# Kernel optimization log

Hardware: AMD Instinct MI355X
Metric: run time of the kernel (lower is better)

## Reference

```python
import jax, jax.numpy as jnp
import numpy as np

H_NODE = 256
H_EDGE = 64
B = 8        # number of graphs
A_PER = 64   # anchors per graph
N_PER = 512  # nodes per graph
INF = 1000000.0
EPS = 1e-8
D_MIN, D_MAX = 0.0, 20.0  # _rbf defaults (gvp-style)


def setup_inputs() -> dict:
    key = jax.random.key(0)
    ks = jax.random.split(key, 16)
    h, he = H_NODE, H_EDGE
    n = lambda k, shp, s=1.0: jax.random.normal(k, shp, jnp.float32) * s
    return {
        "anchor_x": n(ks[0], (B * A_PER, 3), 10.0),
        "node_x": n(ks[1], (B * N_PER, 3), 10.0),
        "anchor_features": n(ks[2], (B * A_PER, h)),
        "node_features": n(ks[3], (B * N_PER, h)),
        "batch": jnp.repeat(jnp.arange(B, dtype=jnp.int32), N_PER),
        "anchor_batch": jnp.repeat(jnp.arange(B, dtype=jnp.int32), A_PER),
        "node_mask": (jax.random.uniform(ks[4], (B * N_PER,)) < 0.9).astype(jnp.float32),
        "Wq": n(ks[5], (h, h), h ** -0.5), "bq": jnp.zeros((h,), jnp.float32),
        "Wkv": n(ks[6], (2 * h, h + he), (h + he) ** -0.5), "bkv": jnp.zeros((2 * h,), jnp.float32),
        "ln1_g": jnp.ones((h,), jnp.float32), "ln1_b": jnp.zeros((h,), jnp.float32),
        "W1": n(ks[7], (2 * h, h), h ** -0.5), "b1": jnp.zeros((2 * h,), jnp.float32),
        "W2": n(ks[8], (2 * h, 2 * h), (2 * h) ** -0.5), "b2": jnp.zeros((2 * h,), jnp.float32),
        "W3": n(ks[9], (h, 2 * h), (2 * h) ** -0.5), "b3": jnp.zeros((h,), jnp.float32),
        "ln2_g": jnp.ones((h,), jnp.float32), "ln2_b": jnp.zeros((h,), jnp.float32),
    }


def _ln(x, g, b, eps=1e-5):
    m = x.mean(-1, keepdims=True)
    v = ((x - m) ** 2).mean(-1, keepdims=True)
    return (x - m) * jax.lax.rsqrt(v + eps) * g + b


def _forward(anchor_x, node_x, anchor_features, node_features, node_mask,
             Wq, bq, Wkv, bkv, ln1_g, ln1_b, W1, b1, W2, b2, W3, b3, ln2_g, ln2_b):
    h, he = H_NODE, H_EDGE
    # equal-sized graphs: reshape global tensors to [B, ., .] (batch ids are repeat(arange(B)))
    q = (anchor_features @ Wq.T + bq).reshape(B, A_PER, h)
    ax = anchor_x.reshape(B, A_PER, 3)
    nx = node_x.reshape(B, N_PER, 3)
    nf = node_features.reshape(B, N_PER, h)
    mask = node_mask.reshape(B, N_PER)

    # pairwise anchor->node distances; original adds scalar eps to the diff vector before the norm
    dist = jnp.linalg.norm(ax[:, :, None, :] - nx[:, None, :, :] + EPS, axis=-1)  # [B,A,N]

    # RBF featurization of dist/10 with D_count = h_edge
    mu = jnp.linspace(D_MIN, D_MAX, he)
    sigma = (D_MAX - D_MIN) / he
    rbf = jnp.exp(-(((dist / 10.0)[..., None] - mu) / sigma) ** 2)  # [B,A,N,he]

    # kv_node(cat([node_feat, rbf])) decomposed: node part computed once per node
    Wkv_n, Wkv_e = Wkv[:, :h], Wkv[:, h:]
    kv_n = nf @ Wkv_n.T + bkv                 # [B,N,2h]
    kv_e = rbf @ Wkv_e.T                      # [B,A,N,2h]
    kv = kv_n[:, None, :, :] + kv_e           # [B,A,N,2h]
    k, v = kv[..., :h], kv[..., h:]

    attn = jnp.einsum('bah,banh->ban', q, k)
    attn = attn * ((mask[:, None, :] - 1.0) * INF)  # faithful to original (multiplicative mask)
    attn = jax.nn.softmax(attn, axis=-1)
    upd = jnp.einsum('ban,banh->bah', attn, v).reshape(B * A_PER, h)

    af = _ln(anchor_features + upd, ln1_g, ln1_b)
    m = jax.nn.relu(af @ W1.T + b1)
    m = jax.nn.relu(m @ W2.T + b2)
    m = m @ W3.T + b3
    return _ln(af + m, ln2_g, ln2_b)


def reference(anchor_x, node_x, anchor_features, node_features, batch, anchor_batch, node_mask,
              Wq, bq, Wkv, bkv, ln1_g, ln1_b, W1, b1, W2, b2, W3, b3, ln2_g, ln2_b):
    # batch / anchor_batch encode equal-sized contiguous graphs; structure is baked into reshapes
    return _forward(anchor_x, node_x, anchor_features, node_features, node_mask,
                    Wq, bq, Wkv, bkv, ln1_g, ln1_b, W1, b1, W2, b2, W3, b3, ln2_g, ln2_b)
```

## Files before the change

kernel.cpp:

```cpp
#include <hip/hip_runtime.h>

#define H    256
#define HE   64
#define NPB  512
#define NA   512
#define MU_STEP (20.0f / 63.0f)
#define INV_SIG 3.2f

__device__ __forceinline__ float wave_sum(float v) {
#pragma unroll
    for (int o = 32; o; o >>= 1) v += __shfl_xor(v, o, 64);
    return v;
}
__device__ __forceinline__ float wave_max(float v) {
#pragma unroll
    for (int o = 32; o; o >>= 1) v = fmaxf(v, __shfl_xor(v, o, 64));
    return v;
}
__device__ __forceinline__ float block_sum1024(float v, float* red16, int t) {
    v = wave_sum(v);
    if ((t & 63) == 0) red16[t >> 6] = v;
    __syncthreads();
    v = 0.f;
#pragma unroll
    for (int i = 0; i < 16; ++i) v += red16[i];
    __syncthreads();
    return v;
}

__global__ void __launch_bounds__(1024) fused_all(
    const float* __restrict__ anchor_x, const float* __restrict__ node_x,
    const float* __restrict__ anchor_f, const float* __restrict__ node_f,
    const float* __restrict__ node_mask,
    const float* __restrict__ Wq,  const float* __restrict__ bq,
    const float* __restrict__ Wkv, const float* __restrict__ bkv,
    const float* __restrict__ ln1_g, const float* __restrict__ ln1_b,
    const float* __restrict__ W1, const float* __restrict__ b1,
    const float* __restrict__ W2, const float* __restrict__ b2,
    const float* __restrict__ W3, const float* __restrict__ b3,
    const float* __restrict__ g2,  const float* __restrict__ bb2,
    float* __restrict__ out)
{
    const int bid = blockIdx.x;
    const int b  = bid & 7;
    const int pr = bid >> 3;
    const int aA = b * 64 + 2 * pr;
    const int aB = aA + 1;
    const int t  = threadIdx.x;
    const int wv = t >> 6, l = t & 63;
    const int sub = l >> 4, kc16 = l & 15;

    __shared__ __align__(16) float qWe_s[2][324];
    __shared__ float q_s[2][256];
    __shared__ float af_s[2][256];
    __shared__ float d10_s[2][NPB];
    __shared__ float mf_s[NPB];
    __shared__ float lg_s[2][NPB];
    __shared__ float w_s[2][NPB];
    __shared__ float snf_s[2][256], rj_s[2][64];
    __shared__ float m1_s[2][512], m2_s[2][512];
    __shared__ float red[512], red16[16];
    __shared__ int   idx_s[2][NPB];
    __shared__ int   cnt_s[2];

    if (t < 256)       af_s[0][t]        = anchor_f[(size_t)aA * 256 + t];
    else if (t < 512)  af_s[1][t - 256]  = anchor_f[(size_t)aB * 256 + (t - 256)];
    if (t < 2) cnt_s[t] = 0;

    if (t < 512) {
        float axA0 = anchor_x[3 * aA], axA1 = anchor_x[3 * aA + 1], axA2 = anchor_x[3 * aA + 2];
        float axB0 = anchor_x[3 * aB], axB1 = anchor_x[3 * aB + 1], axB2 = anchor_x[3 * aB + 2];
        int ng = b * NPB + t;
        float nx0 = node_x[3 * ng], nx1 = node_x[3 * ng + 1], nx2 = node_x[3 * ng + 2];
        float dx = axA0 - nx0 + 1e-8f, dy = axA1 - nx1 + 1e-8f, dz = axA2 - nx2 + 1e-8f;
        d10_s[0][t] = sqrtf(dx * dx + dy * dy + dz * dz) * 0.1f;
        dx = axB0 - nx0 + 1e-8f; dy = axB1 - nx1 + 1e-8f; dz = axB2 - nx2 + 1e-8f;
        d10_s[1][t] = sqrtf(dx * dx + dy * dy + dz * dz) * 0.1f;
        mf_s[t] = (node_mask[ng] - 1.0f) * 1000000.0f;
    }
    __syncthreads();

#pragma unroll
    for (int pass = 0; pass < 4; ++pass) {
        int m = pass * 64 + wv * 4 + sub;
        const float* wr = Wq + (size_t)m * 256 + kc16;
        float w16[16];
#pragma unroll
        for (int v = 0; v < 16; ++v) w16[v] = wr[v * 16];
        float aAc = 0.f, aBc = 0.f;
#pragma unroll
        for (int v = 0; v < 16; ++v) {
            int c = kc16 + v * 16;
            aAc = fmaf(w16[v], af_s[0][c], aAc);
            aBc = fmaf(w16[v], af_s[1][c], aBc);
        }
#pragma unroll
        for (int o = 8; o >= 1; o >>= 1) {
            aAc += __shfl_xor(aAc, o, 64);
            aBc += __shfl_xor(aBc, o, 64);
        }
        if (kc16 == 0) {
            float bv = bq[m];
            q_s[0][m] = aAc + bv;
            q_s[1][m] = aBc + bv;
        }
    }
    __syncthreads();

    {
        int ha = -1, col = 0;
        if (t < 320)                   { ha = 0; col = t; }
        else if (t >= 512 && t < 832)  { ha = 1; col = t - 512; }
        if (ha >= 0) {
            const float* qs = q_s[ha];
            float acc = 0.f;
            for (int o = 0; o < 256; o += 16) {
                float w16[16];
#pragma unroll
                for (int u = 0; u < 16; ++u) w16[u] = Wkv[(size_t)(o + u) * 320 + col];
#pragma unroll
                for (int u = 0; u < 16; ++u) acc = fmaf(w16[u], qs[o + u], acc);
            }
            qWe_s[ha][col] = acc;
        }
    }
    float qbkA = block_sum1024((t < 256) ? q_s[0][t] * bkv[t] : 0.f, red16, t);
    float qbkB = block_sum1024((t < 256) ? q_s[1][t] * bkv[t] : 0.f, red16, t);

    {
        const float4 qA = ((const float4*)qWe_s[0])[l];
        const float4 qB = ((const float4*)qWe_s[1])[l];
        const float qeA = qWe_s[0][256 + l], qeB = qWe_s[1][256 + l];
        const float muL = l * MU_STEP;
        const float4* nfb = (const float4*)(node_f + (size_t)(b * NPB) * 256);

        float4 f0 = nfb[(size_t)wv * 64 + l];
        float4 f1 = nfb[(size_t)(wv + 16) * 64 + l];
        for (int it = 0; it < 32; ++it) {
            const int n = wv + it * 16;
            float4 fn;
            if (it < 30) fn = nfb[(size_t)(n + 32) * 64 + l];

            float sA = qA.x * f0.x + qA.y * f0.y + qA.z * f0.z + qA.w * f0.w;
            float sB = qB.x * f0.x + qB.y * f0.y + qB.z * f0.z + qB.w * f0.w;
            float dA10 = d10_s[0][n], dB10 = d10_s[1][n];
            float u = (dA10 - muL) * INV_SIG; sA = fmaf(qeA, __expf(-u * u), sA);
            u = (dB10 - muL) * INV_SIG;       sB = fmaf(qeB, __expf(-u * u), sB);
#pragma unroll
            for (int o = 1; o < 64; o <<= 1) {
                sA += __shfl_xor(sA, o, 64);
                sB += __shfl_xor(sB, o, 64);
            }
            if (l == 0) {
                lg_s[0][n] = (sA + qbkA) * mf_s[n];
                lg_s[1][n] = (sB + qbkB) * mf_s[n];
            }
            f0 = f1; f1 = fn;
        }
    }
    __syncthreads();

    const int h8 = t >> 9, n9 = t & 511;
    float lg = lg_s[h8][n9];
    {
        float m = wave_max(lg);
        if (l == 0) red16[wv] = m;
    }
    __syncthreads();
    float gmA = red16[0], gmB = red16[8];
#pragma unroll
    for (int i = 1; i < 8; ++i) { gmA = fmaxf(gmA, red16[i]); gmB = fmaxf(gmB, red16[8 + i]); }
    __syncthreads();
    float e = __expf(lg - (h8 ? gmB : gmA));
    w_s[h8][n9] = e;
    {
        float sm = wave_sum(e);
        if (l == 0) red16[wv] = sm;
    }
    __syncthreads();
    float smA = 0.f, smB = 0.f;
#pragma unroll
    for (int i = 0; i < 8; ++i) { smA += red16[i]; smB += red16[8 + i]; }
    const float invA = 1.0f / smA, invB = 1.0f / smB;
    if (e > 0.f) { int p = atomicAdd(&cnt_s[h8], 1); idx_s[h8][p] = n9; }
    __syncthreads();

    if (t < 512) {
        const int hh = t >> 8, col = t & 255;
        const int cnt = cnt_s[hh];
        float s = 0.f;
        const float* base = node_f + (size_t)(b * NPB) * 256 + col;
        for (int i = 0; i < cnt; ++i) {
            int n = idx_s[hh][i];
            s += w_s[hh][n] * base[(size_t)n * 256];
        }
        snf_s[hh][col] = s;
    } else {
        const int tt = t - 512;
        const int ha = tt >> 8, j = tt & 63, g = (tt >> 6) & 3;
        const int cnt = cnt_s[ha];
        float mu = j * MU_STEP;
        float r = 0.f;
        for (int i = g; i < cnt; i += 4) {
            int n = idx_s[ha][i];
            float uu = (d10_s[ha][n] - mu) * INV_SIG;
            r += w_s[ha][n] * __expf(-uu * uu);
        }
        red[tt] = r;
    }
    __syncthreads();
    if (t < 128) {
        int ha = t >> 6, j = t & 63;
        rj_s[ha][j] = red[ha * 256 + j] + red[ha * 256 + 64 + j]
                    + red[ha * 256 + 128 + j] + red[ha * 256 + 192 + j];
    }
    __syncthreads();

#pragma unroll
    for (int pass = 0; pass < 4; ++pass) {
        int m = pass * 64 + wv * 4 + sub;
        const float* wr = Wkv + (size_t)(256 + m) * 320 + kc16;
        float w16[16], w4r[4];
#pragma unroll
        for (int v = 0; v < 16; ++v) w16[v] = wr[v * 16];
#pragma unroll
        for (int v = 0; v < 4; ++v) w4r[v] = wr[256 + v * 16];
        float aAc = 0.f, aBc = 0.f;
#pragma unroll
        for (int v = 0; v < 16; ++v) {
            int c = kc16 + v * 16;
            aAc = fmaf(w16[v], snf_s[0][c], aAc);
            aBc = fmaf(w16[v], snf_s[1][c], aBc);
        }
#pragma unroll
        for (int v = 0; v < 4; ++v) {
            int j = kc16 + v * 16;
            aAc = fmaf(w4r[v], rj_s[0][j], aAc);
            aBc = fmaf(w4r[v], rj_s[1][j], aBc);
        }
#pragma unroll
        for (int o = 8; o >= 1; o >>= 1) {
            aAc += __shfl_xor(aAc, o, 64);
            aBc += __shfl_xor(aBc, o, 64);
        }
        if (kc16 == 0) { red[m] = aAc; red[256 + m] = aBc; }
    }
    __syncthreads();

    const int h = (t >> 8) & 1, th = t & 255;
    float x = 0.f;
    if (t < 512)
        x = af_s[h][th] + red[h * 256 + th] * (h ? invB : invA) + bkv[256 + th];
    {
        float s1 = wave_sum(x);
        if (l == 0) red16[wv] = s1;
    }
    __syncthreads();
    float meanA = (red16[0] + red16[1] + red16[2] + red16[3]) * (1.0f / 256.0f);
    float meanB = (red16[4] + red16[5] + red16[6] + red16[7]) * (1.0f / 256.0f);
    __syncthreads();
    float xc = (t < 512) ? (x - (h ? meanB : meanA)) : 0.f;
    {
        float v1 = wave_sum(xc * xc);
        if (l == 0) red16[wv] = v1;
    }
    __syncthreads();
    float varA = (red16[0] + red16[1] + red16[2] + red16[3]) * (1.0f / 256.0f);
    float varB = (red16[4] + red16[5] + red16[6] + red16[7]) * (1.0f / 256.0f);
    __syncthreads();
    if (t < 512)
        af_s[h][th] = xc * rsqrtf((h ? varB : varA) + 1e-5f) * ln1_g[th] + ln1_b[th];
    __syncthreads();

#pragma unroll
    for (int pass = 0; pass < 8; ++pass) {
        int m = pass * 64 + wv * 4 + sub;
        const float* wr = W1 + (size_t)m * 256 + kc16;
        float w16[16];
#pragma unroll
        for (int v = 0; v < 16; ++v) w16[v] = wr[v * 16];
        float aAc = 0.f, aBc = 0.f;
#pragma unroll
        for (int v = 0; v < 16; ++v) {
            int c = kc16 + v * 16;
            aAc = fmaf(w16[v], af_s[0][c], aAc);
            aBc = fmaf(w16[v], af_s[1][c], aBc);
        }
#pragma unroll
        for (int o = 8; o >= 1; o >>= 1) {
            aAc += __shfl_xor(aAc, o, 64);
            aBc += __shfl_xor(aBc, o, 64);
        }
        if (kc16 == 0) {
            float bv = b1[m];
            m1_s[0][m] = fmaxf(aAc + bv, 0.f);
            m1_s[1][m] = fmaxf(aBc + bv, 0.f);
        }
    }
    __syncthreads();

#pragma unroll
    for (int pass = 0; pass < 8; ++pass) {
        int m = pass * 64 + wv * 4 + sub;
        const float* wr = W2 + (size_t)m * 512 + kc16;
        float aAc = 0.f, aBc = 0.f;
#pragma unroll
        for (int u = 0; u < 32; u += 16) {
            float w16[16];
#pragma unroll
            for (int v = 0; v < 16; ++v) w16[v] = wr[(u + v) * 16];
#pragma unroll
            for (int v = 0; v < 16; ++v) {
                int c = kc16 + (u + v) * 16;
                aAc = fmaf(w16[v], m1_s[0][c], aAc);
                aBc = fmaf(w16[v], m1_s[1][c], aBc);
            }
        }
#pragma unroll
        for (int o = 8; o >= 1; o >>= 1) {
            aAc += __shfl_xor(aAc, o, 64);
            aBc += __shfl_xor(aBc, o, 64);
        }
        if (kc16 == 0) {
            float bv = b2[m];
            m2_s[0][m] = fmaxf(aAc + bv, 0.f);
            m2_s[1][m] = fmaxf(aBc + bv, 0.f);
        }
    }
    __syncthreads();

#pragma unroll
    for (int pass = 0; pass < 4; ++pass) {
        int m = pass * 64 + wv * 4 + sub;
        const float* wr = W3 + (size_t)m * 512 + kc16;
        float aAc = 0.f, aBc = 0.f;
#pragma unroll
        for (int u = 0; u < 32; u += 16) {
            float w16[16];
#pragma unroll
            for (int v = 0; v < 16; ++v) w16[v] = wr[(u + v) * 16];
#pragma unroll
            for (int v = 0; v < 16; ++v) {
                int c = kc16 + (u + v) * 16;
                aAc = fmaf(w16[v], m2_s[0][c], aAc);
                aBc = fmaf(w16[v], m2_s[1][c], aBc);
            }
        }
#pragma unroll
        for (int o = 8; o >= 1; o >>= 1) {
            aAc += __shfl_xor(aAc, o, 64);
            aBc += __shfl_xor(aBc, o, 64);
        }
        if (kc16 == 0) {
            float bv = b3[m];
            red[m]       = aAc + bv;
            red[256 + m] = aBc + bv;
        }
    }
    __syncthreads();

    float y = 0.f;
    if (t < 512) y = red[h * 256 + th] + af_s[h][th];
    {
        float s1 = wave_sum(y);
        if (l == 0) red16[wv] = s1;
    }
    __syncthreads();
    float mnA = (red16[0] + red16[1] + red16[2] + red16[3]) * (1.0f / 256.0f);
    float mnB = (red16[4] + red16[5] + red16[6] + red16[7]) * (1.0f / 256.0f);
    __syncthreads();
    float yc = (t < 512) ? (y - (h ? mnB : mnA)) : 0.f;
    {
        float v1 = wave_sum(yc * yc);
        if (l == 0) red16[wv] = v1;
    }
    __syncthreads();
    float vrA = (red16[0] + red16[1] + red16[2] + red16[3]) * (1.0f / 256.0f);
    float vrB = (red16[4] + red16[5] + red16[6] + red16[7]) * (1.0f / 256.0f);
    if (t < 512) {
        int aOut = h ? aB : aA;
        out[(size_t)aOut * 256 + th] =
            yc * rsqrtf((h ? vrB : vrA) + 1e-5f) * g2[th] + bb2[th];
    }
}

extern "C" void kernel_launch(void* const* d_in, const int* in_sizes, int n_in,
                              void* d_out, int out_size, void* d_ws, size_t ws_size,
                              hipStream_t stream)
{
    const float* anchor_x  = (const float*)d_in[0];
    const float* node_x    = (const float*)d_in[1];
    const float* anchor_f  = (const float*)d_in[2];
    const float* node_f    = (const float*)d_in[3];
    const float* node_mask = (const float*)d_in[6];
    const float* Wq        = (const float*)d_in[7];
    const float* bq        = (const float*)d_in[8];
    const float* Wkv       = (const float*)d_in[9];
    const float* bkv       = (const float*)d_in[10];
    const float* ln1_g     = (const float*)d_in[11];
    const float* ln1_b     = (const float*)d_in[12];
    const float* W1        = (const float*)d_in[13];
    const float* b1        = (const float*)d_in[14];
    const float* W2        = (const float*)d_in[15];
    const float* b2        = (const float*)d_in[16];
    const float* W3        = (const float*)d_in[17];
    const float* b3        = (const float*)d_in[18];
    const float* ln2_g     = (const float*)d_in[19];
    const float* ln2_b     = (const float*)d_in[20];

    fused_all<<<256, 1024, 0, stream>>>(anchor_x, node_x, anchor_f, node_f,
                                        node_mask, Wq, bq, Wkv, bkv,
                                        ln1_g, ln1_b, W1, b1, W2, b2, W3, b3,
                                        ln2_g, ln2_b, (float*)d_out);
}
```

Before: 164.5 us.

## Process one anchor per block and launch 512 blocks instead of 256

Each block previously handled two anchors that shared weight and node-feature loads. Now each block handles a single anchor and the grid doubles to 512 blocks, which fills more of the GPU's compute units (256 CUs on MI355X) at the cost of re-reading the weights and node features twice as often. Shared-memory use per block shrinks, and the launch bounds now request 8 waves per SIMD, which may cap registers per thread. Half of the threads sit idle in several phases, such as the 256-wide layer norms and gathers.

```diff
diff --git a/kernel.cpp b/kernel.cpp
--- a/kernel.cpp
+++ b/kernel.cpp
@@ -28,7 +28,7 @@
     return v;
 }
 
-__global__ void __launch_bounds__(1024) fused_all(
+__global__ void __launch_bounds__(1024, 8) fused_all(
     const float* __restrict__ anchor_x, const float* __restrict__ node_x,
     const float* __restrict__ anchor_f, const float* __restrict__ node_f,
     const float* __restrict__ node_mask,
@@ -42,41 +42,36 @@
     float* __restrict__ out)
 {
     const int bid = blockIdx.x;
-    const int b  = bid & 7;
-    const int pr = bid >> 3;
-    const int aA = b * 64 + 2 * pr;
-    const int aB = aA + 1;
+    const int b = bid & 7;
+    const int a = b * 64 + (bid >> 3);
     const int t  = threadIdx.x;
     const int wv = t >> 6, l = t & 63;
     const int sub = l >> 4, kc16 = l & 15;
 
-    __shared__ __align__(16) float qWe_s[2][324];
-    __shared__ float q_s[2][256];
-    __shared__ float af_s[2][256];
-    __shared__ float d10_s[2][NPB];
+    __shared__ __align__(16) float qWe_s[324];
+    __shared__ float q_s[256];
+    __shared__ float af_s[256];
+    __shared__ float d10_s[NPB];
     __shared__ float mf_s[NPB];
-    __shared__ float lg_s[2][NPB];
-    __shared__ float w_s[2][NPB];
-    __shared__ float snf_s[2][256], rj_s[2][64];
-    __shared__ float m1_s[2][512], m2_s[2][512];
+    __shared__ float lg_s[NPB];
+    __shared__ float w_s[NPB];
+    __shared__ float snf_s[256], rj_s[64];
+    __shared__ float m1_s[512], m2_s[512];
     __shared__ float red[512], red16[16];
-    __shared__ int   idx_s[2][NPB];
-    __shared__ int   cnt_s[2];
-
-    if (t < 256)       af_s[0][t]        = anchor_f[(size_t)aA * 256 + t];
-    else if (t < 512)  af_s[1][t - 256]  = anchor_f[(size_t)aB * 256 + (t - 256)];
-    if (t < 2) cnt_s[t] = 0;
+    __shared__ int   idx_s[NPB];
+    __shared__ int   cnt_s;
+
+    if (t < 256) af_s[t] = anchor_f[(size_t)a * 256 + t];
+    if (t == 0) cnt_s = 0;
 
     if (t < 512) {
-        float axA0 = anchor_x[3 * aA], axA1 = anchor_x[3 * aA + 1], axA2 = anchor_x[3 * aA + 2];
-        float axB0 = anchor_x[3 * aB], axB1 = anchor_x[3 * aB + 1], axB2 = anchor_x[3 * aB + 2];
+        float ax0 = anchor_x[3 * a], ax1 = anchor_x[3 * a + 1], ax2 = anchor_x[3 * a + 2];
         int ng = b * NPB + t;
-        float nx0 = node_x[3 * ng], nx1 = node_x[3 * ng + 1], nx2 = node_x[3 * ng + 2];
-        float dx = axA0 - nx0 + 1e-8f, dy = axA1 - nx1 + 1e-8f, dz = axA2 - nx2 + 1e-8f;
-        d10_s[0][t] = sqrtf(dx * dx + dy * dy + dz * dz) * 0.1f;
-        dx = axB0 - nx0 + 1e-8f; dy = axB1 - nx1 + 1e-8f; dz = axB2 - nx2 + 1e-8f;
-        d10_s[1][t] = sqrtf(dx * dx + dy * dy + dz * dz) * 0.1f;
-        mf_s[t] = (node_mask[ng] - 1.0f) * 1000000.0f;
+        float dx = ax0 - node_x[3 * ng]     + 1e-8f;
+        float dy = ax1 - node_x[3 * ng + 1] + 1e-8f;
+        float dz = ax2 - node_x[3 * ng + 2] + 1e-8f;
+        d10_s[t] = sqrtf(dx * dx + dy * dy + dz * dz) * 0.1f;
+        mf_s[t]  = (node_mask[ng] - 1.0f) * 1000000.0f;
     }
     __syncthreads();
 
@@ -87,50 +82,31 @@
         float w16[16];
 #pragma unroll
         for (int v = 0; v < 16; ++v) w16[v] = wr[v * 16];
-        float aAc = 0.f, aBc = 0.f;
-#pragma unroll
-        for (int v = 0; v < 16; ++v) {
-            int c = kc16 + v * 16;
-            aAc = fmaf(w16[v], af_s[0][c], aAc);
-            aBc = fmaf(w16[v], af_s[1][c], aBc);
-        }
-#pragma unroll
-        for (int o = 8; o >= 1; o >>= 1) {
-            aAc += __shfl_xor(aAc, o, 64);
-            aBc += __shfl_xor(aBc, o, 64);
-        }
-        if (kc16 == 0) {
-            float bv = bq[m];
-            q_s[0][m] = aAc + bv;
-            q_s[1][m] = aBc + bv;
-        }
-    }
-    __syncthreads();
+        float acc = 0.f;
+#pragma unroll
+        for (int v = 0; v < 16; ++v) acc = fmaf(w16[v], af_s[kc16 + v * 16], acc);
+#pragma unroll
+        for (int o = 8; o >= 1; o >>= 1) acc += __shfl_xor(acc, o, 64);
+        if (kc16 == 0) q_s[m] = acc + bq[m];
+    }
+    __syncthreads();
+
+    if (t < 320) {
+        float acc = 0.f;
+        for (int o = 0; o < 256; o += 16) {
+            float w16[16];
+#pragma unroll
+            for (int u = 0; u < 16; ++u) w16[u] = Wkv[(size_t)(o + u) * 320 + t];
+#pragma unroll
+            for (int u = 0; u < 16; ++u) acc = fmaf(w16[u], q_s[o + u], acc);
+        }
+        qWe_s[t] = acc;
+    }
+    const float qbk = block_sum1024((t < 256) ? q_s[t] * bkv[t] : 0.f, red16, t);
 
     {
-        int ha = -1, col = 0;
-        if (t < 320)                   { ha = 0; col = t; }
-        else if (t >= 512 && t < 832)  { ha = 1; col = t - 512; }
-        if (ha >= 0) {
-            const float* qs = q_s[ha];
-            float acc = 0.f;
-            for (int o = 0; o < 256; o += 16) {
-                float w16[16];
-#pragma unroll
-                for (int u = 0; u < 16; ++u) w16[u] = Wkv[(size_t)(o + u) * 320 + col];
-#pragma unroll
-                for (int u = 0; u < 16; ++u) acc = fmaf(w16[u], qs[o + u], acc);
-            }
-            qWe_s[ha][col] = acc;
-        }
-    }
-    float qbkA = block_sum1024((t < 256) ? q_s[0][t] * bkv[t] : 0.f, red16, t);
-    float qbkB = block_sum1024((t < 256) ? q_s[1][t] * bkv[t] : 0.f, red16, t);
-
-    {
-        const float4 qA = ((const float4*)qWe_s[0])[l];
-        const float4 qB = ((const float4*)qWe_s[1])[l];
-        const float qeA = qWe_s[0][256 + l], qeB = qWe_s[1][256 + l];
+        const float4 qA = ((const float4*)qWe_s)[l];
+        const float qeA = qWe_s[256 + l];
         const float muL = l * MU_STEP;
         const float4* nfb = (const float4*)(node_f + (size_t)(b * NPB) * 256);
 
@@ -142,77 +118,68 @@
             if (it < 30) fn = nfb[(size_t)(n + 32) * 64 + l];
 
             float sA = qA.x * f0.x + qA.y * f0.y + qA.z * f0.z + qA.w * f0.w;
-            float sB = qB.x * f0.x + qB.y * f0.y + qB.z * f0.z + qB.w * f0.w;
-            float dA10 = d10_s[0][n], dB10 = d10_s[1][n];
-            float u = (dA10 - muL) * INV_SIG; sA = fmaf(qeA, __expf(-u * u), sA);
-            u = (dB10 - muL) * INV_SIG;       sB = fmaf(qeB, __expf(-u * u), sB);
-#pragma unroll
-            for (int o = 1; o < 64; o <<= 1) {
-                sA += __shfl_xor(sA, o, 64);
-                sB += __shfl_xor(sB, o, 64);
-            }
-            if (l == 0) {
-                lg_s[0][n] = (sA + qbkA) * mf_s[n];
-                lg_s[1][n] = (sB + qbkB) * mf_s[n];
-            }
+            float dA10 = d10_s[n];
+            float u = (dA10 - muL) * INV_SIG;
+            sA = fmaf(qeA, __expf(-u * u), sA);
+#pragma unroll
+            for (int o = 1; o < 64; o <<= 1) sA += __shfl_xor(sA, o, 64);
+            if (l == 0) lg_s[n] = (sA + qbk) * mf_s[n];
             f0 = f1; f1 = fn;
         }
     }
     __syncthreads();
 
-    const int h8 = t >> 9, n9 = t & 511;
-    float lg = lg_s[h8][n9];
+    float lg = (t < 512) ? lg_s[t] : -3.4e38f;
     {
         float m = wave_max(lg);
         if (l == 0) red16[wv] = m;
     }
     __syncthreads();
-    float gmA = red16[0], gmB = red16[8];
-#pragma unroll
-    for (int i = 1; i < 8; ++i) { gmA = fmaxf(gmA, red16[i]); gmB = fmaxf(gmB, red16[8 + i]); }
-    __syncthreads();
-    float e = __expf(lg - (h8 ? gmB : gmA));
-    w_s[h8][n9] = e;
+    float gm = red16[0];
+#pragma unroll
+    for (int i = 1; i < 16; ++i) gm = fmaxf(gm, red16[i]);
+    __syncthreads();
+    float e = (t < 512) ? __expf(lg - gm) : 0.f;
+    if (t < 512) w_s[t] = e;
     {
         float sm = wave_sum(e);
         if (l == 0) red16[wv] = sm;
     }
     __syncthreads();
-    float smA = 0.f, smB = 0.f;
-#pragma unroll
-    for (int i = 0; i < 8; ++i) { smA += red16[i]; smB += red16[8 + i]; }
-    const float invA = 1.0f / smA, invB = 1.0f / smB;
-    if (e > 0.f) { int p = atomicAdd(&cnt_s[h8], 1); idx_s[h8][p] = n9; }
-    __syncthreads();
-
-    if (t < 512) {
-        const int hh = t >> 8, col = t & 255;
-        const int cnt = cnt_s[hh];
+    float sm = 0.f;
+#pragma unroll
+    for (int i = 0; i < 16; ++i) sm += red16[i];
+    const float inv = 1.0f / sm;
+    if (t < 512 && e > 0.f) { int p = atomicAdd(&cnt_s, 1); idx_s[p] = t; }
+    __syncthreads();
+    const int cnt = cnt_s;
+
+    if (t < 256) {
         float s = 0.f;
-        const float* base = node_f + (size_t)(b * NPB) * 256 + col;
+        const float* base = node_f + (size_t)(b * NPB) * 256 + t;
         for (int i = 0; i < cnt; ++i) {
-            int n = idx_s[hh][i];
-            s += w_s[hh][n] * base[(size_t)n * 256];
-        }
-        snf_s[hh][col] = s;
-    } else {
+            int n = idx_s[i];
+            s += w_s[n] * base[(size_t)n * 256];
+        }
+        snf_s[t] = s;
+    } else if (t >= 512) {
         const int tt = t - 512;
-        const int ha = tt >> 8, j = tt & 63, g = (tt >> 6) & 3;
-        const int cnt = cnt_s[ha];
+        const int j = tt & 63, g = tt >> 6;
         float mu = j * MU_STEP;
         float r = 0.f;
-        for (int i = g; i < cnt; i += 4) {
-            int n = idx_s[ha][i];
-            float uu = (d10_s[ha][n] - mu) * INV_SIG;
-            r += w_s[ha][n] * __expf(-uu * uu);
+        for (int i = g; i < cnt; i += 8) {
+            int n = idx_s[i];
+            float uu = (d10_s[n] - mu) * INV_SIG;
+            r += w_s[n] * __expf(-uu * uu);
         }
         red[tt] = r;
     }
     __syncthreads();
-    if (t < 128) {
-        int ha = t >> 6, j = t & 63;
-        rj_s[ha][j] = red[ha * 256 + j] + red[ha * 256 + 64 + j]
-                    + red[ha * 256 + 128 + j] + red[ha * 256 + 192 + j];
+    if (t < 64) {
+        float r = 0.f;
+#pragma unroll
+        for (int g = 0; g < 8; ++g) r += red[t + 64 * g];
+        rj_s[t] = r;
     }
     __syncthreads();
 
@@ -225,51 +192,24 @@
         for (int v = 0; v < 16; ++v) w16[v] = wr[v * 16];
 #pragma unroll
         for (int v = 0; v < 4; ++v) w4r[v] = wr[256 + v * 16];
-        float aAc = 0.f, aBc = 0.f;
-#pragma unroll
-        for (int v = 0; v < 16; ++v) {
-            int c = kc16 + v * 16;
-            aAc = fmaf(w16[v], snf_s[0][c], aAc);
-            aBc = fmaf(w16[v], snf_s[1][c], aBc);
-        }
-#pragma unroll
-        for (int v = 0; v < 4; ++v) {
-            int j = kc16 + v * 16;
-            aAc = fmaf(w4r[v], rj_s[0][j], aAc);
-            aBc = fmaf(w4r[v], rj_s[1][j], aBc);
-        }
-#pragma unroll
-        for (int o = 8; o >= 1; o >>= 1) {
-            aAc += __shfl_xor(aAc, o, 64);
-            aBc += __shfl_xor(aBc, o, 64);
-        }
-        if (kc16 == 0) { red[m] = aAc; red[256 + m] = aBc; }
-    }
-    __syncthreads();
-
-    const int h = (t >> 8) & 1, th = t & 255;
+        float acc = 0.f;
+#pragma unroll
+        for (int v = 0; v < 16; ++v) acc = fmaf(w16[v], snf_s[kc16 + v * 16], acc);
+#pragma unroll
+        for (int v = 0; v < 4; ++v) acc = fmaf(w4r[v], rj_s[kc16 + v * 16], acc);
+#pragma unroll
+        for (int o = 8; o >= 1; o >>= 1) acc += __shfl_xor(acc, o, 64);
+        if (kc16 == 0) red[m] = acc;
+    }
+    __syncthreads();
+
     float x = 0.f;
-    if (t < 512)
-        x = af_s[h][th] + red[h * 256 + th] * (h ? invB : invA) + bkv[256 + th];
-    {
-        float s1 = wave_sum(x);
-        if (l == 0) red16[wv] = s1;
-    }
-    __syncthreads();
-    float meanA = (red16[0] + red16[1] + red16[2] + red16[3]) * (1.0f / 256.0f);
-    float meanB = (red16[4] + red16[5] + red16[6] + red16[7]) * (1.0f / 256.0f);
-    __syncthreads();
-    float xc = (t < 512) ? (x - (h ? meanB : meanA)) : 0.f;
-    {
-        float v1 = wave_sum(xc * xc);
-        if (l == 0) red16[wv] = v1;
-    }
-    __syncthreads();
-    float varA = (red16[0] + red16[1] + red16[2] + red16[3]) * (1.0f / 256.0f);
-    float varB = (red16[4] + red16[5] + red16[6] + red16[7]) * (1.0f / 256.0f);
-    __syncthreads();
-    if (t < 512)
-        af_s[h][th] = xc * rsqrtf((h ? varB : varA) + 1e-5f) * ln1_g[th] + ln1_b[th];
+    if (t < 256) x = af_s[t] + red[t] * inv + bkv[256 + t];
+    float mean = block_sum1024(x, red16, t) * (1.0f / 256.0f);
+    float xc = (t < 256) ? (x - mean) : 0.f;
+    float var = block_sum1024(xc * xc, red16, t) * (1.0f / 256.0f);
+    if (t < 256)
+        af_s[t] = xc * rsqrtf(var + 1e-5f) * ln1_g[t] + ln1_b[t];
     __syncthreads();
 
 #pragma unroll
@@ -279,23 +219,12 @@
         float w16[16];
 #pragma unroll
         for (int v = 0; v < 16; ++v) w16[v] = wr[v * 16];
-        float aAc = 0.f, aBc = 0.f;
-#pragma unroll
-        for (int v = 0; v < 16; ++v) {
-            int c = kc16 + v * 16;
-            aAc = fmaf(w16[v], af_s[0][c], aAc);
-            aBc = fmaf(w16[v], af_s[1][c], aBc);
-        }
-#pragma unroll
-        for (int o = 8; o >= 1; o >>= 1) {
-            aAc += __shfl_xor(aAc, o, 64);
-            aBc += __shfl_xor(aBc, o, 64);
-        }
-        if (kc16 == 0) {
-            float bv = b1[m];
-            m1_s[0][m] = fmaxf(aAc + bv, 0.f);
-            m1_s[1][m] = fmaxf(aBc + bv, 0.f);
-        }
+        float acc = 0.f;
+#pragma unroll
+        for (int v = 0; v < 16; ++v) acc = fmaf(w16[v], af_s[kc16 + v * 16], acc);
+#pragma unroll
+        for (int o = 8; o >= 1; o >>= 1) acc += __shfl_xor(acc, o, 64);
+        if (kc16 == 0) m1_s[m] = fmaxf(acc + b1[m], 0.f);
     }
     __syncthreads();
 
@@ -303,29 +232,19 @@
     for (int pass = 0; pass < 8; ++pass) {
         int m = pass * 64 + wv * 4 + sub;
         const float* wr = W2 + (size_t)m * 512 + kc16;
-        float aAc = 0.f, aBc = 0.f;
+        float acc = 0.f;
 #pragma unroll
         for (int u = 0; u < 32; u += 16) {
             float w16[16];
 #pragma unroll
             for (int v = 0; v < 16; ++v) w16[v] = wr[(u + v) * 16];
 #pragma unroll
-            for (int v = 0; v < 16; ++v) {
-                int c = kc16 + (u + v) * 16;
-                aAc = fmaf(w16[v], m1_s[0][c], aAc);
-                aBc = fmaf(w16[v], m1_s[1][c], aBc);
-            }
-        }
-#pragma unroll
-        for (int o = 8; o >= 1; o >>= 1) {
-            aAc += __shfl_xor(aAc, o, 64);
-            aBc += __shfl_xor(aBc, o, 64);
-        }
-        if (kc16 == 0) {
-            float bv = b2[m];
-            m2_s[0][m] = fmaxf(aAc + bv, 0.f);
-            m2_s[1][m] = fmaxf(aBc + bv, 0.f);
-        }
+            for (int v = 0; v < 16; ++v)
+                acc = fmaf(w16[v], m1_s[kc16 + (u + v) * 16], acc);
+        }
+#pragma unroll
+        for (int o = 8; o >= 1; o >>= 1) acc += __shfl_xor(acc, o, 64);
+        if (kc16 == 0) m2_s[m] = fmaxf(acc + b2[m], 0.f);
     }
     __syncthreads();
 
@@ -333,55 +252,29 @@
     for (int pass = 0; pass < 4; ++pass) {
         int m = pass * 64 + wv * 4 + sub;
         const float* wr = W3 + (size_t)m * 512 + kc16;
-        float aAc = 0.f, aBc = 0.f;
+        float acc = 0.f;
 #pragma unroll
         for (int u = 0; u < 32; u += 16) {
             float w16[16];
 #pragma unroll
             for (int v = 0; v < 16; ++v) w16[v] = wr[(u + v) * 16];
 #pragma unroll
-            for (int v = 0; v < 16; ++v) {
-                int c = kc16 + (u + v) * 16;
-                aAc = fmaf(w16[v], m2_s[0][c], aAc);
-                aBc = fmaf(w16[v], m2_s[1][c], aBc);
-            }
-        }
-#pragma unroll
-        for (int o = 8; o >= 1; o >>= 1) {
-            aAc += __shfl_xor(aAc, o, 64);
-            aBc += __shfl_xor(aBc, o, 64);
-        }
-        if (kc16 == 0) {
-            float bv = b3[m];
-            red[m]       = aAc + bv;
-            red[256 + m] = aBc + bv;
-        }
+            for (int v = 0; v < 16; ++v)
+                acc = fmaf(w16[v], m2_s[kc16 + (u + v) * 16], acc);
+        }
+#pragma unroll
+        for (int o = 8; o >= 1; o >>= 1) acc += __shfl_xor(acc, o, 64);
+        if (kc16 == 0) red[m] = acc + b3[m];
     }
     __syncthreads();
 
     float y = 0.f;
-    if (t < 512) y = red[h * 256 + th] + af_s[h][th];
-    {
-        float s1 = wave_sum(y);
-        if (l == 0) red16[wv] = s1;
-    }
-    __syncthreads();
-    float mnA = (red16[0] + red16[1] + red16[2] + red16[3]) * (1.0f / 256.0f);
-    float mnB = (red16[4] + red16[5] + red16[6] + red16[7]) * (1.0f / 256.0f);
-    __syncthreads();
-    float yc = (t < 512) ? (y - (h ? mnB : mnA)) : 0.f;
-    {
-        float v1 = wave_sum(yc * yc);
-        if (l == 0) red16[wv] = v1;
-    }
-    __syncthreads();
-    float vrA = (red16[0] + red16[1] + red16[2] + red16[3]) * (1.0f / 256.0f);
-    float vrB = (red16[4] + red16[5] + red16[6] + red16[7]) * (1.0f / 256.0f);
-    if (t < 512) {
-        int aOut = h ? aB : aA;
-        out[(size_t)aOut * 256 + th] =
-            yc * rsqrtf((h ? vrB : vrA) + 1e-5f) * g2[th] + bb2[th];
-    }
+    if (t < 256) y = red[t] + af_s[t];
+    float mn = block_sum1024(y, red16, t) * (1.0f / 256.0f);
+    float yc = (t < 256) ? (y - mn) : 0.f;
+    float vr = block_sum1024(yc * yc, red16, t) * (1.0f / 256.0f);
+    if (t < 256)
+        out[(size_t)a * 256 + t] = yc * rsqrtf(vr + 1e-5f) * g2[t] + bb2[t];
 }
 
 extern "C" void kernel_launch(void* const* d_in, const int* in_sizes, int n_in,
@@ -408,8 +301,8 @@
     const float* ln2_g     = (const float*)d_in[19];
     const float* ln2_b     = (const float*)d_in[20];
 
-    fused_all<<<256, 1024, 0, stream>>>(anchor_x, node_x, anchor_f, node_f,
-                                        node_mask, Wq, bq, Wkv, bkv,
-                                        ln1_g, ln1_b, W1, b1, W2, b2, W3, b3,
-                                        ln2_g, ln2_b, (float*)d_out);
-}
+    fused_all<<<NA, 1024, 0, stream>>>(anchor_x, node_x, anchor_f, node_f,
+                                       node_mask, Wq, bq, Wkv, bkv,
+                                       ln1_g, ln1_b, W1, b1, W2, b2, W3, b3,
+                                       ln2_g, ln2_b, (float*)d_out);
+}
```

Result: slower. 188.3 us (+14.4%).
